# Kernel tuning notes

Measured on AMD Instinct MI355X. Metric: run time of the kernel, lower is better.

## Reference

```python
import jax, jax.numpy as jnp
import numpy as np

IN_C = 64
K = 3          # kernel_size
PAD = K // 2   # padding for offset_conv and deformconv


def conv2d(x, w, b, pad):
    # x: [B,C,H,W], w: [O,I,kh,kw] (OIHW), stride 1
    y = jax.lax.conv_general_dilated(
        x, w, (1, 1), [(pad, pad), (pad, pad)],
        dimension_numbers=('NCHW', 'OIHW', 'NCHW'))
    return y + b[None, :, None, None]


def deform_conv2d(x, offset, w, b, pad):
    # torchvision DeformConv2d (v1, no modulation), stride=1, dilation=1.
    # x: [B,Cin,H,W]; offset: [B,2*K*K,H,W] as (dy,dx) pairs per kernel tap
    # (row-major tap order); w: [Cout,Cin,K,K]; b: [Cout].
    B, Cin, H, W = x.shape
    Kh = w.shape[-1]
    K2 = Kh * Kh
    off = offset.reshape(B, K2, 2, H, W)
    dy, dx = off[:, :, 0], off[:, :, 1]                     # [B,K2,H,W]

    ky = (jnp.arange(K2) // Kh).astype(x.dtype)             # kernel tap rows
    kx = (jnp.arange(K2) % Kh).astype(x.dtype)              # kernel tap cols
    base_y = jnp.arange(H, dtype=x.dtype)[None, :, None] - pad + ky[:, None, None]  # [K2,H,1]
    base_x = jnp.arange(W, dtype=x.dtype)[None, None, :] - pad + kx[:, None, None]  # [K2,1,W]
    py = base_y[None] + dy                                  # [B,K2,H,W] sample y
    px = base_x[None] + dx                                  # [B,K2,H,W] sample x

    y0 = jnp.floor(py)
    x0 = jnp.floor(px)
    wy1 = py - y0; wy0 = 1.0 - wy1                          # bilinear weights
    wx1 = px - x0; wx0 = 1.0 - wx1

    x_flat = x.reshape(B, Cin, H * W)

    def gather(iy, ix):
        # zero-padded bilinear corner gather -> [B,Cin,K2,H,W]
        valid = (iy >= 0) & (iy < H) & (ix >= 0) & (ix < W)
        iyc = jnp.clip(iy, 0, H - 1).astype(jnp.int32)
        ixc = jnp.clip(ix, 0, W - 1).astype(jnp.int32)
        flat = (iyc * W + ixc).reshape(B, -1)               # [B,K2*H*W]
        g = jax.vmap(lambda xb, ib: xb[:, ib])(x_flat, flat)
        g = g.reshape(B, Cin, K2, H, W)
        return g * valid.reshape(B, 1, K2, H, W).astype(x.dtype)

    val = (gather(y0,       x0      ) * (wy0 * wx0)[:, None]
         + gather(y0,       x0 + 1.0) * (wy0 * wx1)[:, None]
         + gather(y0 + 1.0, x0      ) * (wy1 * wx0)[:, None]
         + gather(y0 + 1.0, x0 + 1.0) * (wy1 * wx1)[:, None])  # [B,Cin,K2,H,W]

    out = jnp.einsum('bckhw,ock->bohw', val, w.reshape(w.shape[0], Cin, K2))
    return out + b[None, :, None, None]


def setup_inputs() -> dict:
    key = jax.random.key(0)
    ks = jax.random.split(key, 7)
    B, H, W = 2, 256, 256
    f32 = jnp.float32
    x = jax.random.normal(ks[0], (B, IN_C, H, W), f32)
    # ConvTranspose2d weight layout: [in_c, out_c=64, K, K]
    w_deconv = jax.random.normal(ks[1], (IN_C, 64, K, K), f32) * 0.05
    b_deconv = jax.random.normal(ks[2], (64,), f32) * 0.05
    w_off = jax.random.normal(ks[3], (2 * K * K, 64, K, K), f32) * 0.05
    b_off = jax.random.normal(ks[4], (2 * K * K,), f32) * 0.05
    w_def = jax.random.normal(ks[5], (IN_C, 64, K, K), f32) * 0.05
    b_def = jax.random.normal(ks[6], (IN_C,), f32) * 0.05
    return {'x': x, 'w_deconv': w_deconv, 'b_deconv': b_deconv,
            'w_off': w_off, 'b_off': b_off, 'w_def': w_def, 'b_def': b_def}


def reference(x, w_deconv, b_deconv, w_off, b_off, w_def, b_def):
    # ConvTranspose2d(stride=1, pad=1) == conv with flipped, IO-transposed
    # weights and padding K-1-1 = 1.
    wt = jnp.flip(w_deconv, (2, 3)).transpose(1, 0, 2, 3)   # [64, in_c, K, K]
    h = jax.nn.relu(conv2d(x, wt, b_deconv, K - 1 - 1))
    offset = conv2d(h, w_off, b_off, PAD)
    out = deform_conv2d(h, offset, w_def, b_def, PAD)
    return jax.nn.relu(out)
```

## Files before the change

kernel.cpp:

```cpp
#include <hip/hip_runtime.h>

#define H_ 256
#define W_ 256
#define HW_ (H_*W_)

typedef __attribute__((ext_vector_type(8))) short bf16x8;
typedef __attribute__((ext_vector_type(4))) float f32x4;
typedef __attribute__((ext_vector_type(2))) float f32x2;

__device__ __forceinline__ float bflo(unsigned u) { return __builtin_bit_cast(float, u << 16); }
__device__ __forceinline__ float bfhi(unsigned u) { return __builtin_bit_cast(float, u & 0xffff0000u); }
__device__ __forceinline__ unsigned f2bf(float f) {
    unsigned b = __builtin_bit_cast(unsigned, f);
    b += 0x7fffu + ((b >> 16) & 1u);
    return b >> 16;
}
__device__ __forceinline__ unsigned cvtpk(float lo, float hi) {
    unsigned r;
    asm("v_cvt_pk_bf16_f32 %0, %1, %2" : "=v"(r) : "v"(lo), "v"(hi));
    return r;
}
__device__ __forceinline__ void unpack8(uint4 v, float* f) {
    f[0] = bflo(v.x); f[1] = bfhi(v.x); f[2] = bflo(v.y); f[3] = bfhi(v.y);
    f[4] = bflo(v.z); f[5] = bfhi(v.z); f[6] = bflo(v.w); f[7] = bfhi(v.w);
}
__device__ __forceinline__ f32x2 pair2(unsigned u) {
    f32x2 r;
    r[0] = bflo(u); r[1] = bfhi(u);
    return r;
}

__global__ void prep_weights(const float* __restrict__ wdef, unsigned short* __restrict__ wdefb,
                             const float* __restrict__ wdc, unsigned short* __restrict__ wdcb,
                             const float* __restrict__ woff, unsigned short* __restrict__ woffb) {
    int idx = blockIdx.x * 256 + threadIdx.x;
    if (idx < 36864) {
        int k = idx >> 12, o = (idx >> 6) & 63, c = idx & 63;
        wdefb[idx] = (unsigned short)f2bf(wdef[(o * 64 + c) * 9 + k]);
        wdcb[idx]  = (unsigned short)f2bf(wdc[(c * 64 + o) * 9 + (8 - k)]);
    }
    if (idx < 18432) {
        int k = idx >> 11, o = (idx >> 6) & 31, c = idx & 63;
        woffb[idx] = (o < 18) ? (unsigned short)f2bf(woff[(o * 64 + c) * 9 + k])
                              : (unsigned short)0;
    }
}

__global__ __launch_bounds__(256) void x_to_nhwc(const float* __restrict__ x,
                                                 unsigned short* __restrict__ xb) {
    __shared__ unsigned short t[64 * 72];
    int tid = threadIdx.x;
    int b = blockIdx.x >> 10;
    long pxb = (long)(blockIdx.x & 1023) * 64;
    const float* xp = x + (long)b * 64 * HW_ + pxb;
    int px = tid & 63, cg = tid >> 6;
    for (int c = cg; c < 64; c += 4)
        t[px * 72 + c] = (unsigned short)f2bf(xp[(long)c * HW_ + px]);
    __syncthreads();
    int spx = tid >> 2, q = tid & 3;
    unsigned short* dst = xb + ((long)b * HW_ + pxb + spx) * 64 + q * 16;
    *(uint4*)dst       = *(const uint4*)&t[spx * 72 + q * 16];
    *(uint4*)(dst + 8) = *(const uint4*)&t[spx * 72 + q * 16 + 8];
}

__global__ __launch_bounds__(256, 4) void conv1_mfma(const unsigned short* __restrict__ xb,
                                                     const unsigned short* __restrict__ wdcb,
                                                     const float* __restrict__ bias,
                                                     unsigned short* __restrict__ h) {
    __shared__ __align__(16) unsigned short sA[2][130 * 72];

    int tid = threadIdx.x;
    int linear = (blockIdx.x & 7) * 128 + (blockIdx.x >> 3);
    int bx = linear & 1;
    int y  = (linear >> 1) & 255;
    int b  = linear >> 9;
    int X0 = bx * 128;

    int wave = tid >> 6, lane = tid & 63;
    int lr = lane & 15, lg = lane >> 4;
    int n0 = wave * 16;

    f32x4 acc[8];
#pragma unroll
    for (int m = 0; m < 8; ++m) { acc[m][0]=0.f; acc[m][1]=0.f; acc[m][2]=0.f; acc[m][3]=0.f; }

    const unsigned short* xbb = xb + (long)b * HW_ * 64;
    const unsigned short* pb  = wdcb + (n0 + lr) * 64 + lg * 8;

    int r0 = (y == 0) ? 1 : 0;
    int r1 = (y == H_ - 1) ? 1 : 2;

    uint4 L[5];
    auto LOADROW = [&](int yr) {
        const unsigned short* src = xbb + (long)yr * (W_ * 64);
#pragma unroll
        for (int t = 0; t < 5; ++t) {
            int e = tid + t * 256;
            uint4 v = { 0u, 0u, 0u, 0u };
            if (e < 1040) {
                int col = X0 - 1 + (e >> 3);
                if (col >= 0 && col < W_)
                    v = *(const uint4*)&src[(long)col * 64 + (e & 7) * 8];
            }
            L[t] = v;
        }
    };

    LOADROW(y + r0 - 1);
    int pa = 0;
    for (int ky = r0; ky <= r1; ++ky, ++pa) {
        unsigned short* buf = sA[pa & 1];
#pragma unroll
        for (int t = 0; t < 5; ++t) {
            int e = tid + t * 256;
            if (e < 1040) *(uint4*)&buf[(e >> 3) * 72 + (e & 7) * 8] = L[t];
        }
        if (ky < r1) LOADROW(y + ky);
        asm volatile("s_waitcnt lgkmcnt(0)" ::: "memory");
        __builtin_amdgcn_s_barrier();
        asm volatile("" ::: "memory");
#pragma unroll
        for (int kx = 0; kx < 3; ++kx) {
            int k = ky * 3 + kx;
            bf16x8 b0 = *(const bf16x8*)(pb + k * 4096);
            bf16x8 b1 = *(const bf16x8*)(pb + k * 4096 + 32);
#pragma unroll
            for (int m = 0; m < 8; ++m) {
                const unsigned short* ap = &buf[(m * 16 + lr + kx) * 72 + lg * 8];
                bf16x8 a0 = *(const bf16x8*)ap;
                bf16x8 a1 = *(const bf16x8*)(ap + 32);
                acc[m] = __builtin_amdgcn_mfma_f32_16x16x32_bf16(a0, b0, acc[m], 0, 0, 0);
                acc[m] = __builtin_amdgcn_mfma_f32_16x16x32_bf16(a1, b1, acc[m], 0, 0, 0);
            }
        }
    }

    __syncthreads();
    float bv = bias[n0 + lr];
    unsigned short* cs = sA[0];
#pragma unroll
    for (int m = 0; m < 8; ++m)
#pragma unroll
        for (int r = 0; r < 4; ++r) {
            float vv = fmaxf(acc[m][r] + bv, 0.f);
            cs[(m * 16 + lg * 4 + r) * 72 + n0 + lr] = (unsigned short)f2bf(vv);
        }
    __syncthreads();
    int spx = tid >> 1, sc0 = (tid & 1) * 32;
    unsigned short* dst = h + ((long)b * HW_ + (long)y * W_ + X0 + spx) * 64 + sc0;
    const unsigned short* srcp = &cs[spx * 72 + sc0];
#pragma unroll
    for (int q = 0; q < 4; ++q)
        *(uint4*)(dst + q * 8) = *(const uint4*)(srcp + q * 8);
}

__global__ __launch_bounds__(256, 4) void conv2_mfma(const unsigned short* __restrict__ h,
                                                     const unsigned short* __restrict__ woffb,
                                                     const float* __restrict__ bias,
                                                     float* __restrict__ off) {
    __shared__ __align__(16) unsigned short sA[2][130 * 72];

    int tid = threadIdx.x;
    int linear = (blockIdx.x & 7) * 128 + (blockIdx.x >> 3);
    int bx = linear & 1;
    int y  = (linear >> 1) & 255;
    int b  = linear >> 9;
    int X0 = bx * 128;

    int wave = tid >> 6, lane = tid & 63;
    int lr = lane & 15, lg = lane >> 4;
    int pxh = wave & 1, nh = wave >> 1;
    int n0 = nh * 16;
    int pxb = pxh * 64;

    f32x4 acc[4];
#pragma unroll
    for (int m = 0; m < 4; ++m) { acc[m][0]=0.f; acc[m][1]=0.f; acc[m][2]=0.f; acc[m][3]=0.f; }

    const unsigned short* hb = h + (long)b * HW_ * 64;
    const unsigned short* pb = woffb + (n0 + lr) * 64 + lg * 8;

    int r0 = (y == 0) ? 1 : 0;
    int r1 = (y == H_ - 1) ? 1 : 2;

    uint4 L[5];
    auto LOADROW = [&](int yr) {
        const unsigned short* src = hb + (long)yr * (W_ * 64);
#pragma unroll
        for (int t = 0; t < 5; ++t) {
            int e = tid + t * 256;
            uint4 v = { 0u, 0u, 0u, 0u };
            if (e < 1040) {
                int col = X0 - 1 + (e >> 3);
                if (col >= 0 && col < W_)
                    v = *(const uint4*)&src[(long)col * 64 + (e & 7) * 8];
            }
            L[t] = v;
        }
    };

    LOADROW(y + r0 - 1);
    int pa = 0;
    for (int ky = r0; ky <= r1; ++ky, ++pa) {
        unsigned short* buf = sA[pa & 1];
#pragma unroll
        for (int t = 0; t < 5; ++t) {
            int e = tid + t * 256;
            if (e < 1040) *(uint4*)&buf[(e >> 3) * 72 + (e & 7) * 8] = L[t];
        }
        if (ky < r1) LOADROW(y + ky);
        asm volatile("s_waitcnt lgkmcnt(0)" ::: "memory");
        __builtin_amdgcn_s_barrier();
        asm volatile("" ::: "memory");
#pragma unroll
        for (int kx = 0; kx < 3; ++kx) {
            int k = ky * 3 + kx;
            bf16x8 b0 = *(const bf16x8*)(pb + k * 2048);
            bf16x8 b1 = *(const bf16x8*)(pb + k * 2048 + 32);
#pragma unroll
            for (int m = 0; m < 4; ++m) {
                const unsigned short* ap = &buf[(pxb + m * 16 + lr + kx) * 72 + lg * 8];
                bf16x8 a0 = *(const bf16x8*)ap;
                bf16x8 a1 = *(const bf16x8*)(ap + 32);
                acc[m] = __builtin_amdgcn_mfma_f32_16x16x32_bf16(a0, b0, acc[m], 0, 0, 0);
                acc[m] = __builtin_amdgcn_mfma_f32_16x16x32_bf16(a1, b1, acc[m], 0, 0, 0);
            }
        }
    }

    int o = n0 + lr;
    if (o < 18) {
        float bv = bias[o];
        float* op = off + ((long)b * 18 + o) * HW_ + (long)y * W_ + X0 + pxb;
#pragma unroll
        for (int m = 0; m < 4; ++m) {
            float4 r = { acc[m][0] + bv, acc[m][1] + bv, acc[m][2] + bv, acc[m][3] + bv };
            *(float4*)(op + m * 16 + lg * 4) = r;
        }
    }
}

struct Pass16 {
    uint4 a00, a01, a10, a11;
    uint4 b00, b01, b10, b11;
    float w00, w01, w10, w11;
};

__device__ __forceinline__ Pass16 issue16(const unsigned short* __restrict__ hb,
                                          int k, int y, int px, float dy, float dx, int c0) {
    Pass16 s;
    float py  = (float)(y - 1 + k / 3) + dy;
    float pxs = (float)(px - 1 + k % 3) + dx;
    float y0f = floorf(py), x0f = floorf(pxs);
    int iy0 = (int)y0f, ix0 = (int)x0f;
    float wy1 = py - y0f, wx1 = pxs - x0f;
    float wy0 = 1.f - wy1, wx0 = 1.f - wx1;
    bool vy0 = (iy0 >= 0) && (iy0 < H_);
    bool vy1 = (iy0 >= -1) && (iy0 < H_ - 1);
    bool vx0 = (ix0 >= 0) && (ix0 < W_);
    bool vx1 = (ix0 >= -1) && (ix0 < W_ - 1);
    int cy0 = min(max(iy0, 0), H_ - 1), cy1 = min(max(iy0 + 1, 0), H_ - 1);
    int cx0 = min(max(ix0, 0), W_ - 1), cx1 = min(max(ix0 + 1, 0), W_ - 1);
    s.w00 = wy0 * wx0 * ((vy0 && vx0) ? 1.f : 0.f);
    s.w01 = wy0 * wx1 * ((vy0 && vx1) ? 1.f : 0.f);
    s.w10 = wy1 * wx0 * ((vy1 && vx0) ? 1.f : 0.f);
    s.w11 = wy1 * wx1 * ((vy1 && vx1) ? 1.f : 0.f);
    int r00 = (cy0 * W_ + cx0) * 64 + c0, r01 = (cy0 * W_ + cx1) * 64 + c0;
    int r10 = (cy1 * W_ + cx0) * 64 + c0, r11 = (cy1 * W_ + cx1) * 64 + c0;
    s.a00 = *(const uint4*)&hb[r00];     s.a01 = *(const uint4*)&hb[r01];
    s.a10 = *(const uint4*)&hb[r10];     s.a11 = *(const uint4*)&hb[r11];
    s.b00 = *(const uint4*)&hb[r00 + 8]; s.b01 = *(const uint4*)&hb[r01 + 8];
    s.b10 = *(const uint4*)&hb[r10 + 8]; s.b11 = *(const uint4*)&hb[r11 + 8];
    return s;
}

__device__ __forceinline__ uint4 interp8p(uint4 q0, uint4 q1, uint4 q2, uint4 q3,
                                          f32x2 w00, f32x2 w01, f32x2 w10, f32x2 w11) {
    const unsigned* u0 = (const unsigned*)&q0;
    const unsigned* u1 = (const unsigned*)&q1;
    const unsigned* u2 = (const unsigned*)&q2;
    const unsigned* u3 = (const unsigned*)&q3;
    unsigned r[4];
#pragma unroll
    for (int j = 0; j < 4; ++j) {
        f32x2 v = pair2(u0[j]) * w00;
        v = __builtin_elementwise_fma(pair2(u1[j]), w01, v);
        v = __builtin_elementwise_fma(pair2(u2[j]), w10, v);
        v = __builtin_elementwise_fma(pair2(u3[j]), w11, v);
        r[j] = cvtpk(v[0], v[1]);
    }
    uint4 u = { r[0], r[1], r[2], r[3] };
    return u;
}

__global__ __launch_bounds__(256, 5) void deform_mfma(const unsigned short* __restrict__ h,
                                                      const float* __restrict__ off,
                                                      const unsigned short* __restrict__ wdefb,
                                                      const float* __restrict__ bias,
                                                      float* __restrict__ out) {
    __shared__ __align__(16) unsigned short val[2][64 * 64];

    int tid = threadIdx.x;
    int linear = (blockIdx.x & 7) * 256 + (blockIdx.x >> 3);
    int b  = linear >> 10;
    int y  = (linear >> 2) & 255;
    int x0 = (linear & 3) * 64;

    int lane = tid & 63, wave = tid >> 6;
    int lr = lane & 15, lg = lane >> 4;
    int n0 = wave * 16;
    int gpx = tid >> 2;
    int gc  = tid & 3;
    int c0  = gc * 16;
    int gx  = x0 + gpx;

    f32x4 acc[4];
#pragma unroll
    for (int m = 0; m < 4; ++m) { acc[m][0]=0.f; acc[m][1]=0.f; acc[m][2]=0.f; acc[m][3]=0.f; }

    const unsigned short* hb   = h + (long)b * HW_ * 64;
    const float* ofb  = off + (long)b * 18 * HW_ + y * W_ + gx;
    const unsigned short* bsrc = wdefb + (n0 + lr) * 64 + lg * 8;

    float dy0 = ofb[0], dx0 = ofb[HW_];
    Pass16 S = issue16(hb, 0, y, gx, dy0, dx0, c0);
    float dyn = ofb[2 * HW_], dxn = ofb[3 * HW_];

    int slotL = ((2 * gc)     ^ (gpx & 7)) * 8;
    int slotH = ((2 * gc + 1) ^ (gpx & 7)) * 8;
    int rdL   = ((lg)     ^ (lr & 7)) * 8;
    int rdH   = ((lg + 4) ^ (lr & 7)) * 8;

    for (int k = 0; k < 9; ++k) {
        bf16x8 bc0 = *(const bf16x8*)(bsrc + k * 4096);
        bf16x8 bc1 = *(const bf16x8*)(bsrc + k * 4096 + 32);

        f32x2 v00 = { S.w00, S.w00 }, v01 = { S.w01, S.w01 };
        f32x2 v10 = { S.w10, S.w10 }, v11 = { S.w11, S.w11 };
        unsigned short* vb = val[k & 1];
        *(uint4*)&vb[gpx * 64 + slotL] = interp8p(S.a00, S.a01, S.a10, S.a11,
                                                  v00, v01, v10, v11);
        *(uint4*)&vb[gpx * 64 + slotH] = interp8p(S.b00, S.b01, S.b10, S.b11,
                                                  v00, v01, v10, v11);

        asm volatile("s_waitcnt lgkmcnt(0)" ::: "memory");
        __builtin_amdgcn_s_barrier();
        asm volatile("" ::: "memory");

        Pass16 S2;
        float dy3 = 0.f, dx3 = 0.f;
        if (k < 8) {
            S2 = issue16(hb, k + 1, y, gx, dyn, dxn, c0);
            if (k < 7) { dy3 = ofb[(2 * k + 4) * HW_]; dx3 = ofb[(2 * k + 5) * HW_]; }
        }
        __builtin_amdgcn_sched_barrier(0);

        __builtin_amdgcn_s_setprio(1);
#pragma unroll
        for (int m = 0; m < 4; ++m) {
            const unsigned short* ap = &vb[(m * 16 + lr) * 64];
            bf16x8 a0 = *(const bf16x8*)&ap[rdL];
            bf16x8 a1 = *(const bf16x8*)&ap[rdH];
            acc[m] = __builtin_amdgcn_mfma_f32_16x16x32_bf16(a0, bc0, acc[m], 0, 0, 0);
            acc[m] = __builtin_amdgcn_mfma_f32_16x16x32_bf16(a1, bc1, acc[m], 0, 0, 0);
        }
        __builtin_amdgcn_s_setprio(0);

        S = S2; dyn = dy3; dxn = dx3;
    }

    float bv = bias[n0 + lr];
    float* outb = out + ((long)b * 64 + n0 + lr) * HW_ + y * W_ + x0;
#pragma unroll
    for (int m = 0; m < 4; ++m) {
        float4 r = { fmaxf(acc[m][0] + bv, 0.f), fmaxf(acc[m][1] + bv, 0.f),
                     fmaxf(acc[m][2] + bv, 0.f), fmaxf(acc[m][3] + bv, 0.f) };
        *(float4*)(outb + m * 16 + lg * 4) = r;
    }
}

extern "C" void kernel_launch(void* const* d_in, const int* in_sizes, int n_in,
                              void* d_out, int out_size, void* d_ws, size_t ws_size,
                              hipStream_t stream) {
    const float* x        = (const float*)d_in[0];
    const float* w_deconv = (const float*)d_in[1];
    const float* b_deconv = (const float*)d_in[2];
    const float* w_off    = (const float*)d_in[3];
    const float* b_off    = (const float*)d_in[4];
    const float* w_def    = (const float*)d_in[5];
    const float* b_def    = (const float*)d_in[6];
    float* out = (float*)d_out;

    char* ws = (char*)d_ws;
    unsigned short* xbb   = (unsigned short*)ws;
    unsigned short* hbf   = (unsigned short*)(ws + 16777216);
    float* offset         = (float*)(ws + 33554432);
    unsigned short* wdcb  = (unsigned short*)(ws + 42991616);
    unsigned short* wdefb = (unsigned short*)(ws + 43065344);
    unsigned short* woffb = (unsigned short*)(ws + 43139072);

    prep_weights<<<144, 256, 0, stream>>>(w_def, wdefb, w_deconv, wdcb, w_off, woffb);
    x_to_nhwc<<<2048, 256, 0, stream>>>(x, xbb);
    conv1_mfma<<<1024, 256, 0, stream>>>(xbb, wdcb, b_deconv, hbf);
    conv2_mfma<<<1024, 256, 0, stream>>>(hbf, woffb, b_off, offset);
    deform_mfma<<<2048, 256, 0, stream>>>(hbf, offset, wdefb, b_def, out);
}
```

Measured before the change: 95.55 us.

## Process deform taps in pairs with batched gathers instead of software prefetch

```diff
diff --git a/kernel.cpp b/kernel.cpp
--- a/kernel.cpp
+++ b/kernel.cpp
@@ -19,10 +19,6 @@
     unsigned r;
     asm("v_cvt_pk_bf16_f32 %0, %1, %2" : "=v"(r) : "v"(lo), "v"(hi));
     return r;
-}
-__device__ __forceinline__ void unpack8(uint4 v, float* f) {
-    f[0] = bflo(v.x); f[1] = bfhi(v.x); f[2] = bflo(v.y); f[3] = bfhi(v.y);
-    f[4] = bflo(v.z); f[5] = bfhi(v.z); f[6] = bflo(v.w); f[7] = bfhi(v.w);
 }
 __device__ __forceinline__ f32x2 pair2(unsigned u) {
     f32x2 r;
@@ -293,12 +289,12 @@
     return u;
 }
 
-__global__ __launch_bounds__(256, 5) void deform_mfma(const unsigned short* __restrict__ h,
+__global__ __launch_bounds__(256, 4) void deform_mfma(const unsigned short* __restrict__ h,
                                                       const float* __restrict__ off,
                                                       const unsigned short* __restrict__ wdefb,
                                                       const float* __restrict__ bias,
                                                       float* __restrict__ out) {
-    __shared__ __align__(16) unsigned short val[2][64 * 64];
+    __shared__ __align__(16) unsigned short val[2][2][64 * 64];
 
     int tid = threadIdx.x;
     int linear = (blockIdx.x & 7) * 256 + (blockIdx.x >> 3);
@@ -322,51 +318,83 @@
     const float* ofb  = off + (long)b * 18 * HW_ + y * W_ + gx;
     const unsigned short* bsrc = wdefb + (n0 + lr) * 64 + lg * 8;
 
-    float dy0 = ofb[0], dx0 = ofb[HW_];
-    Pass16 S = issue16(hb, 0, y, gx, dy0, dx0, c0);
-    float dyn = ofb[2 * HW_], dxn = ofb[3 * HW_];
+    float dyA = ofb[0],        dxA = ofb[HW_];
+    float dyB = ofb[2 * HW_],  dxB = ofb[3 * HW_];
 
     int slotL = ((2 * gc)     ^ (gpx & 7)) * 8;
     int slotH = ((2 * gc + 1) ^ (gpx & 7)) * 8;
     int rdL   = ((lg)     ^ (lr & 7)) * 8;
     int rdH   = ((lg + 4) ^ (lr & 7)) * 8;
 
-    for (int k = 0; k < 9; ++k) {
-        bf16x8 bc0 = *(const bf16x8*)(bsrc + k * 4096);
-        bf16x8 bc1 = *(const bf16x8*)(bsrc + k * 4096 + 32);
-
-        f32x2 v00 = { S.w00, S.w00 }, v01 = { S.w01, S.w01 };
-        f32x2 v10 = { S.w10, S.w10 }, v11 = { S.w11, S.w11 };
-        unsigned short* vb = val[k & 1];
-        *(uint4*)&vb[gpx * 64 + slotL] = interp8p(S.a00, S.a01, S.a10, S.a11,
-                                                  v00, v01, v10, v11);
-        *(uint4*)&vb[gpx * 64 + slotH] = interp8p(S.b00, S.b01, S.b10, S.b11,
-                                                  v00, v01, v10, v11);
+    for (int kp = 0; kp < 9; kp += 2) {
+        int pb = (kp >> 1) & 1;
+        bool has2 = (kp + 1 < 9);
+
+        bf16x8 bc0 = *(const bf16x8*)(bsrc + kp * 4096);
+        bf16x8 bc1 = *(const bf16x8*)(bsrc + kp * 4096 + 32);
+        bf16x8 bd0 = bc0, bd1 = bc1;
+        if (has2) {
+            bd0 = *(const bf16x8*)(bsrc + (kp + 1) * 4096);
+            bd1 = *(const bf16x8*)(bsrc + (kp + 1) * 4096 + 32);
+        }
+
+        Pass16 S0 = issue16(hb, kp, y, gx, dyA, dxA, c0);
+        Pass16 S1;
+        if (has2) S1 = issue16(hb, kp + 1, y, gx, dyB, dxB, c0);
+
+        float dyn0 = 0.f, dxn0 = 0.f, dyn1 = 0.f, dxn1 = 0.f;
+        if (kp + 2 < 9) { dyn0 = ofb[(2 * kp + 4) * HW_]; dxn0 = ofb[(2 * kp + 5) * HW_]; }
+        if (kp + 3 < 9) { dyn1 = ofb[(2 * kp + 6) * HW_]; dxn1 = ofb[(2 * kp + 7) * HW_]; }
+
+        {
+            f32x2 w00 = { S0.w00, S0.w00 }, w01 = { S0.w01, S0.w01 };
+            f32x2 w10 = { S0.w10, S0.w10 }, w11 = { S0.w11, S0.w11 };
+            unsigned short* vb = val[pb][0];
+            *(uint4*)&vb[gpx * 64 + slotL] = interp8p(S0.a00, S0.a01, S0.a10, S0.a11,
+                                                      w00, w01, w10, w11);
+            *(uint4*)&vb[gpx * 64 + slotH] = interp8p(S0.b00, S0.b01, S0.b10, S0.b11,
+                                                      w00, w01, w10, w11);
+        }
+        if (has2) {
+            f32x2 w00 = { S1.w00, S1.w00 }, w01 = { S1.w01, S1.w01 };
+            f32x2 w10 = { S1.w10, S1.w10 }, w11 = { S1.w11, S1.w11 };
+            unsigned short* vb = val[pb][1];
+            *(uint4*)&vb[gpx * 64 + slotL] = interp8p(S1.a00, S1.a01, S1.a10, S1.a11,
+                                                      w00, w01, w10, w11);
+            *(uint4*)&vb[gpx * 64 + slotH] = interp8p(S1.b00, S1.b01, S1.b10, S1.b11,
+                                                      w00, w01, w10, w11);
+        }
 
         asm volatile("s_waitcnt lgkmcnt(0)" ::: "memory");
         __builtin_amdgcn_s_barrier();
         asm volatile("" ::: "memory");
 
-        Pass16 S2;
-        float dy3 = 0.f, dx3 = 0.f;
-        if (k < 8) {
-            S2 = issue16(hb, k + 1, y, gx, dyn, dxn, c0);
-            if (k < 7) { dy3 = ofb[(2 * k + 4) * HW_]; dx3 = ofb[(2 * k + 5) * HW_]; }
-        }
-        __builtin_amdgcn_sched_barrier(0);
-
         __builtin_amdgcn_s_setprio(1);
-#pragma unroll
-        for (int m = 0; m < 4; ++m) {
-            const unsigned short* ap = &vb[(m * 16 + lr) * 64];
-            bf16x8 a0 = *(const bf16x8*)&ap[rdL];
-            bf16x8 a1 = *(const bf16x8*)&ap[rdH];
-            acc[m] = __builtin_amdgcn_mfma_f32_16x16x32_bf16(a0, bc0, acc[m], 0, 0, 0);
-            acc[m] = __builtin_amdgcn_mfma_f32_16x16x32_bf16(a1, bc1, acc[m], 0, 0, 0);
+        {
+            const unsigned short* vb = val[pb][0];
+#pragma unroll
+            for (int m = 0; m < 4; ++m) {
+                const unsigned short* ap = &vb[(m * 16 + lr) * 64];
+                bf16x8 a0 = *(const bf16x8*)&ap[rdL];
+                bf16x8 a1 = *(const bf16x8*)&ap[rdH];
+                acc[m] = __builtin_amdgcn_mfma_f32_16x16x32_bf16(a0, bc0, acc[m], 0, 0, 0);
+                acc[m] = __builtin_amdgcn_mfma_f32_16x16x32_bf16(a1, bc1, acc[m], 0, 0, 0);
+            }
+        }
+        if (has2) {
+            const unsigned short* vb = val[pb][1];
+#pragma unroll
+            for (int m = 0; m < 4; ++m) {
+                const unsigned short* ap = &vb[(m * 16 + lr) * 64];
+                bf16x8 a0 = *(const bf16x8*)&ap[rdL];
+                bf16x8 a1 = *(const bf16x8*)&ap[rdH];
+                acc[m] = __builtin_amdgcn_mfma_f32_16x16x32_bf16(a0, bd0, acc[m], 0, 0, 0);
+                acc[m] = __builtin_amdgcn_mfma_f32_16x16x32_bf16(a1, bd1, acc[m], 0, 0, 0);
+            }
         }
         __builtin_amdgcn_s_setprio(0);
 
-        S = S2; dyn = dy3; dxn = dx3;
+        dyA = dyn0; dxA = dxn0; dyB = dyn1; dxB = dxn1;
     }
 
     float bv = bias[n0 + lr];
```

Measured after the change: 97.59 us. 2.1% more time.
